# Performance work log

Hardware: AMD Instinct MI355X
Metric: run time of the kernel (lower is better)

The kernel has to match this reference:

```python
import jax, jax.numpy as jnp
import numpy as np

B, NPER, F, D, E, NUM_STEPS = 256, 512, 256, 32, 524288, 4
N = B * NPER
INIT_TAU, TAU_SCALE, STEP_ALPHA = 0.1, 0.5, 5.0


def setup_inputs() -> dict:
    key = jax.random.key(0)
    ks = jax.random.split(key, 10)
    x_start = jax.random.uniform(ks[0], (N,), jnp.float32, 0.1, 1.0)   # strictly positive iterate
    x_solution = jax.random.uniform(ks[1], (N,), jnp.float32, 0.0, 1.0)
    q = jax.random.normal(ks[2], (N,), jnp.float32)
    edge_src = jax.random.randint(ks[3], (E,), 0, N, jnp.int32)
    edge_dst = jax.random.randint(ks[4], (E,), 0, N, jnp.int32)
    vals_batch = jnp.repeat(jnp.arange(B, dtype=jnp.int32), NPER)      # equal-sized graphs
    proj_matrix = jax.random.normal(ks[5], (B, NPER, F), jnp.float32) / np.float32(np.sqrt(NPER))
    W_in = jax.random.normal(ks[6], (2, D), jnp.float32) / np.float32(np.sqrt(2.0))
    b_in = jnp.zeros((D,), jnp.float32)
    W_msg = jax.random.normal(ks[7], (D, D), jnp.float32) / np.float32(np.sqrt(D))
    b_msg = jnp.zeros((D,), jnp.float32)
    W_out = jax.random.normal(ks[8], (D, 1), jnp.float32) / np.float32(np.sqrt(D))
    b_out = jnp.zeros((1,), jnp.float32)
    return {"x_start": x_start, "x_solution": x_solution, "q": q,
            "proj_matrix": proj_matrix, "W_in": W_in, "b_in": b_in,
            "W_msg": W_msg, "b_msg": b_msg, "W_out": W_out, "b_out": b_out,
            "edge_src": edge_src, "edge_dst": edge_dst, "vals_batch": vals_batch}


def _l1_normalize(x, batch):
    # per-graph L1 normalization: x / sum_i |x_i| over the graph segment
    s = jax.ops.segment_sum(jnp.abs(x), batch, num_segments=B)
    return x / (s[batch] + 1e-12)


def _line_search(x, d, batch, max_alpha):
    # largest per-graph alpha s.t. x + alpha*d >= 0, capped at max_alpha
    ratio = jnp.where(d < 0, x / jnp.maximum(-d, 1e-12), max_alpha)
    a = jnp.clip(jax.ops.segment_min(ratio, batch, num_segments=B), 0.0, max_alpha)
    return a[batch]  # gathered back to per-node


def _gnn(xs, q, edge_src, edge_dst, W_in, b_in, W_msg, b_msg, W_out, b_out):
    h = jax.nn.relu(jnp.stack([xs, q], axis=-1) @ W_in + b_in)      # [N, D]
    m = h[edge_src] @ W_msg + b_msg                                  # [E, D]
    agg = jax.ops.segment_sum(m, edge_dst, num_segments=N)          # [N, D]
    h2 = jax.nn.relu(h + agg)
    return h2 @ W_out[:, 0] + b_out[0]                               # [N]


def reference(x_start, x_solution, q, proj_matrix, W_in, b_in, W_msg, b_msg,
              W_out, b_out, edge_src, edge_dst, vals_batch):
    tau = INIT_TAU
    xs = x_start
    preds, labels = [], []
    for _ in range(NUM_STEPS):
        pred = _gnn(xs, q, edge_src, edge_dst, W_in, b_in, W_msg, b_msg, W_out, b_out)
        preds.append(pred)
        labels.append(_l1_normalize(x_solution - xs, vals_batch))
        p = _l1_normalize(jax.lax.stop_gradient(pred), vals_batch)   # .detach() in torch
        direction = p + 3.0 * tau / (xs + tau)
        tau = max(tau * TAU_SCALE, 1e-5)
        # to_dense_batch with equal graph sizes == reshape; project onto nullspace basis
        dd = direction.reshape(B, NPER)
        df = jnp.einsum('bnf,bn->bf', proj_matrix, dd)               # [B, F]
        pproj = jnp.einsum('bnf,bf->bn', proj_matrix, df).reshape(-1)  # [N]
        alpha = _line_search(xs, pproj, vals_batch, STEP_ALPHA) * 0.995
        xs = xs + alpha * pproj
    return jnp.stack(preds, axis=1), jnp.stack(labels, axis=1)       # each [N, NUM_STEPS]
```

## Files before the change

kernel.cpp:

```cpp
#include <hip/hip_runtime.h>

#define BB 256
#define NPER 512
#define FF 256
#define DD 32
#define EE 524288
#define NN (BB*NPER)
#define NSTEPS 4

__device__ __forceinline__ float bflo(unsigned u) { return __uint_as_float(u << 16); }
__device__ __forceinline__ float bfhi(unsigned u) { return __uint_as_float(u & 0xFFFF0000u); }
__device__ __forceinline__ unsigned rtn_bf16(unsigned u) {
    return (u + 0x7FFFu + ((u >> 16) & 1u)) >> 16;
}


__global__ void k_degpack(const int* __restrict__ dst, unsigned* __restrict__ deg,
                          const float* __restrict__ xs0, const float* __restrict__ q,
                          float2* __restrict__ xq) {
    int t = blockIdx.x * blockDim.x + threadIdx.x;
    if (t < NN) { float2 v; v.x = xs0[t]; v.y = q[t]; xq[t] = v; }
    atomicAdd(&deg[dst[t]], 1u);
}

__global__ __launch_bounds__(256) void k_alloc(const unsigned* __restrict__ deg,
                                               unsigned* __restrict__ gcur,
                                               unsigned* __restrict__ rowstart,
                                               unsigned* __restrict__ cursor) {
    __shared__ unsigned r[256];
    __shared__ unsigned base;
    int t = threadIdx.x;
    int i = blockIdx.x * 256 + t;
    unsigned d = deg[i];
    r[t] = d;
    __syncthreads();
    for (int o = 1; o < 256; o <<= 1) {
        unsigned v = (t >= o) ? r[t - o] : 0u;
        __syncthreads();
        r[t] += v;
        __syncthreads();
    }
    if (t == 255) base = atomicAdd(gcur, r[255]);
    __syncthreads();
    unsigned excl = r[t] - d + base;
    rowstart[i] = excl;
    cursor[i] = excl;
}

__global__ void k_fill(const int* __restrict__ src, const int* __restrict__ dst,
                       unsigned* __restrict__ cursor, int* __restrict__ csr_src) {
    int e = blockIdx.x * blockDim.x + threadIdx.x;
    unsigned pos = atomicAdd(&cursor[dst[e]], 1u);
    csr_src[pos] = src[e];
}


template<int STEP>
__global__ void k_node_g(const float2* __restrict__ xq,
                         const float* __restrict__ Win, const float* __restrict__ bin,
                         const unsigned* __restrict__ rowstart, const unsigned* __restrict__ deg,
                         const int* __restrict__ csr_src,
                         const float* __restrict__ Wmsg, const float* __restrict__ bmsg,
                         const float* __restrict__ Wout, const float* __restrict__ bout,
                         float* __restrict__ pred, float* __restrict__ out_preds) {
    int tid = threadIdx.x;
    int d = tid & 31;
    int i = blockIdx.x * 8 + (tid >> 5);
    float w0 = Win[d], w1 = Win[DD + d], b0 = bin[d];
    float wcol[DD];
    #pragma unroll
    for (int k = 0; k < DD; ++k) wcol[k] = Wmsg[k * DD + d];
    unsigned rs = rowstart[i];
    unsigned dg = deg[i];
    unsigned nfull = dg < 32u ? dg : 32u;
    float xv = 0.f, qv = 0.f;
    if ((unsigned)d < nfull) {
        int sv = csr_src[rs + d];
        float2 v = xq[sv];
        xv = v.x; qv = v.y;
    }
    float s = 0.f;
    for (unsigned j = 0; j < nfull; ++j) {
        float xj = __shfl(xv, (int)j, 32);
        float qj = __shfl(qv, (int)j, 32);
        s += fmaxf(xj * w0 + qj * w1 + b0, 0.f);
    }
    for (unsigned j = 32; j < dg; ++j) {
        int sv = csr_src[rs + j];
        float2 v = xq[sv];
        s += fmaxf(v.x * w0 + v.y * w1 + b0, 0.f);
    }
    float2 self = xq[i];
    float hval = fmaxf(self.x * w0 + self.y * w1 + b0, 0.f);
    float agg = (float)dg * bmsg[d];
    #pragma unroll
    for (int k = 0; k < DD; ++k) agg += __shfl(s, k, 32) * wcol[k];
    float h2 = fmaxf(hval + agg, 0.f);
    float v = h2 * Wout[d];
    for (int o = 16; o > 0; o >>= 1) v += __shfl_down(v, o, 32);
    if (d == 0) {
        float pr = v + bout[0];
        pred[i] = pr;
        out_preds[i * NSTEPS + STEP] = pr;
    }
}

template<int STEP0>
__global__ __launch_bounds__(256) void k_dfc(const float* __restrict__ Pf,
                                             unsigned short* __restrict__ Pbf,
                                             const float2* __restrict__ xq,
                                             const float* __restrict__ xsol,
                                             const float* __restrict__ pred,
                                             float* __restrict__ out_labels,
                                             float* __restrict__ dfp,
                                             float tau, int step) {
    __shared__ float dd_l[64];
    __shared__ float sl[4 * FF];
    __shared__ float redA[4], redB[4];
    int blk = blockIdx.x;
    int b = blk >> 3, s = blk & 7;
    int t = threadIdx.x;
    int w = t >> 6, lane = t & 63;
    int gbase = b * NPER;

    float x0 = xq[gbase + t].x;
    float x1 = xq[gbase + 256 + t].x;
    float r0 = xsol[gbase + t] - x0;
    float r1 = xsol[gbase + 256 + t] - x1;
    float a1 = fabsf(r0) + fabsf(r1);
    float a2 = fabsf(pred[gbase + t]) + fabsf(pred[gbase + 256 + t]);
    #pragma unroll
    for (int o = 32; o > 0; o >>= 1) {
        a1 += __shfl_down(a1, o, 64);
        a2 += __shfl_down(a2, o, 64);
    }
    if (lane == 0) { redA[w] = a1; redB[w] = a2; }
    __syncthreads();
    float Sr = 1e-12f + redA[0] + redA[1] + redA[2] + redA[3];
    float Sp = 1e-12f + redB[0] + redB[1] + redB[2] + redB[3];
    if (s == 0) {
        out_labels[(size_t)(gbase + t) * NSTEPS + step] = r0 / Sr;
        out_labels[(size_t)(gbase + 256 + t) * NSTEPS + step] = r1 / Sr;
    }
    if (t < 64) {
        int row = s * 64 + t;
        float xx = xq[gbase + row].x;
        dd_l[t] = pred[gbase + row] / Sp + 3.0f * tau / (xx + tau);
    }
    __syncthreads();

    size_t pbase = ((size_t)(gbase + s * 64 + w * 16)) * FF + 4 * lane;
    float4 acc = {0.f, 0.f, 0.f, 0.f};
    if (STEP0) {
        const float4* Pr = (const float4*)(Pf + pbase);
        uint2* Pw = (uint2*)(Pbf + pbase);
        #pragma unroll 4
        for (int n = 0; n < 16; ++n) {
            float4 pv = Pr[(size_t)n * 64];
            float sc = dd_l[w * 16 + n];
            acc.x += pv.x * sc; acc.y += pv.y * sc;
            acc.z += pv.z * sc; acc.w += pv.w * sc;
            unsigned u0 = rtn_bf16(__float_as_uint(pv.x));
            unsigned u1 = rtn_bf16(__float_as_uint(pv.y));
            unsigned u2 = rtn_bf16(__float_as_uint(pv.z));
            unsigned u3 = rtn_bf16(__float_as_uint(pv.w));
            uint2 o; o.x = u0 | (u1 << 16); o.y = u2 | (u3 << 16);
            Pw[(size_t)n * 64] = o;
        }
    } else {
        const uint2* Pr = (const uint2*)(Pbf + pbase);
        #pragma unroll 8
        for (int n = 0; n < 16; ++n) {
            uint2 pv = Pr[(size_t)n * 64];
            float sc = dd_l[w * 16 + n];
            acc.x += bflo(pv.x) * sc; acc.y += bfhi(pv.x) * sc;
            acc.z += bflo(pv.y) * sc; acc.w += bfhi(pv.y) * sc;
        }
    }
    ((float4*)sl)[w * 64 + lane] = acc;
    __syncthreads();
    if (t < FF) {
        float v = sl[t] + sl[FF + t] + sl[2 * FF + t] + sl[3 * FF + t];
        dfp[(size_t)((step * BB + b) * 8 + s) * FF + t] = v;
    }
}

__global__ __launch_bounds__(1024) void k_ppu(const unsigned short* __restrict__ Pbf,
                                              const float* __restrict__ dfp,
                                              float2* __restrict__ xq,
                                              const float* __restrict__ xsol,
                                              float* __restrict__ out_labels,
                                              int step, int last) {
    __shared__ float x_l[NPER], pp_l[NPER], dfl[FF];
    __shared__ float wmin[16], red[16];
    int b = blockIdx.x;
    int t = threadIdx.x;
    int w = t >> 6, lane = t & 63;
    int gbase = b * NPER;
    if (t < FF) {
        const float* dp = dfp + (size_t)((step * BB + b) * 8) * FF + t;
        float v = 0.f;
        #pragma unroll
        for (int s = 0; s < 8; ++s) v += dp[s * FF];
        dfl[t] = v;
    }
    if (t < NPER) x_l[t] = xq[gbase + t].x;
    __syncthreads();

    float4 dfv = ((const float4*)dfl)[lane];
    const uint2* Pr = (const uint2*)(Pbf + ((size_t)(gbase + w * 32)) * FF + 4 * lane);
    float mloc = 5.0f;
    #pragma unroll
    for (int n = 0; n < 32; ++n) {
        uint2 pv = Pr[(size_t)n * 64];
        float pr = bflo(pv.x) * dfv.x + bfhi(pv.x) * dfv.y
                 + bflo(pv.y) * dfv.z + bfhi(pv.y) * dfv.w;
        #pragma unroll
        for (int o = 1; o < 64; o <<= 1) pr += __shfl_xor(pr, o, 64);
        int row = w * 32 + n;
        if (lane == 0) pp_l[row] = pr;
        float ratio = (pr < 0.f) ? (x_l[row] / fmaxf(-pr, 1e-12f)) : 5.0f;
        mloc = fminf(mloc, ratio);
    }
    if (lane == 0) wmin[w] = mloc;
    __syncthreads();
    float mm = wmin[0];
    #pragma unroll
    for (int k = 1; k < 16; ++k) mm = fminf(mm, wmin[k]);
    float alpha = fminf(fmaxf(mm, 0.f), 5.0f) * 0.995f;
    float xnew = 0.f;
    if (t < NPER) {
        xnew = x_l[t] + alpha * pp_l[t];
        xq[gbase + t].x = xnew;
    }
    if (last) {
        float r = 0.f, a1 = 0.f;
        if (t < NPER) { r = xsol[gbase + t] - xnew; a1 = fabsf(r); }
        #pragma unroll
        for (int o = 32; o > 0; o >>= 1) a1 += __shfl_down(a1, o, 64);
        if (lane == 0) red[w] = a1;
        __syncthreads();
        float Sr = 1e-12f;
        #pragma unroll
        for (int k = 0; k < 16; ++k) Sr += red[k];
        if (t < NPER) out_labels[(size_t)(gbase + t) * NSTEPS + (NSTEPS - 1)] = r / Sr;
    }
}


extern "C" void kernel_launch(void* const* d_in, const int* in_sizes, int n_in,
                              void* d_out, int out_size, void* d_ws, size_t ws_size,
                              hipStream_t stream) {
    const float* x_start = (const float*)d_in[0];
    const float* x_sol   = (const float*)d_in[1];
    const float* q       = (const float*)d_in[2];
    const float* P       = (const float*)d_in[3];
    const float* Win     = (const float*)d_in[4];
    const float* bin     = (const float*)d_in[5];
    const float* Wmsg    = (const float*)d_in[6];
    const float* bmsg    = (const float*)d_in[7];
    const float* Wout    = (const float*)d_in[8];
    const float* bout    = (const float*)d_in[9];
    const int*   esrc    = (const int*)d_in[10];
    const int*   edst    = (const int*)d_in[11];

    float* out_preds  = (float*)d_out;
    float* out_labels = (float*)d_out + (size_t)NN * NSTEPS;

    float* w = (float*)d_ws;
    unsigned* deg  = (unsigned*)w; w += NN;
    unsigned* gcur = (unsigned*)w; w += 2;
    float2* xq  = (float2*)w; w += 2 * (size_t)NN;
    float* pred  = w; w += NN;
    float* dfp   = w; w += (size_t)3 * BB * 8 * FF;
    unsigned* rowstart = (unsigned*)w; w += NN;
    unsigned* cursor   = (unsigned*)w; w += NN;
    int* csr_src       = (int*)w;      w += EE;
    unsigned short* Pbf = (unsigned short*)w;

    hipMemsetAsync(deg, 0, (NN + 2) * sizeof(unsigned), stream);
    k_degpack<<<EE / 256, 256, 0, stream>>>(edst, deg, x_start, q, xq);
    k_alloc<<<NN / 256, 256, 0, stream>>>(deg, gcur, rowstart, cursor);
    k_fill<<<EE / 256, 256, 0, stream>>>(esrc, edst, cursor, csr_src);

    float tau = 0.1f;
    for (int step = 0; step < NSTEPS; ++step) {
        switch (step) {
        case 0: k_node_g<0><<<NN / 8, 256, 0, stream>>>(xq, Win, bin, rowstart, deg, csr_src,
                                                        Wmsg, bmsg, Wout, bout, pred, out_preds); break;
        case 1: k_node_g<1><<<NN / 8, 256, 0, stream>>>(xq, Win, bin, rowstart, deg, csr_src,
                                                        Wmsg, bmsg, Wout, bout, pred, out_preds); break;
        case 2: k_node_g<2><<<NN / 8, 256, 0, stream>>>(xq, Win, bin, rowstart, deg, csr_src,
                                                        Wmsg, bmsg, Wout, bout, pred, out_preds); break;
        default: k_node_g<3><<<NN / 8, 256, 0, stream>>>(xq, Win, bin, rowstart, deg, csr_src,
                                                         Wmsg, bmsg, Wout, bout, pred, out_preds); break;
        }
        if (step < NSTEPS - 1) {
            if (step == 0)
                k_dfc<1><<<BB * 8, 256, 0, stream>>>(P, Pbf, xq, x_sol, pred,
                                                     out_labels, dfp, tau, step);
            else
                k_dfc<0><<<BB * 8, 256, 0, stream>>>(P, Pbf, xq, x_sol, pred,
                                                     out_labels, dfp, tau, step);
            k_ppu<<<BB, 1024, 0, stream>>>(Pbf, dfp, xq, x_sol, out_labels,
                                           step, step == NSTEPS - 2 ? 1 : 0);
        }
        tau = fmaxf(tau * 0.5f, 1e-5f);
    }
}
```

Measured before the change: 527.3 us.

## Fuse projection and back-projection kernels, keeping P rows in registers

```diff
diff --git a/kernel.cpp b/kernel.cpp
--- a/kernel.cpp
+++ b/kernel.cpp
@@ -106,29 +106,29 @@
 }
 
 template<int STEP0>
-__global__ __launch_bounds__(256) void k_dfc(const float* __restrict__ Pf,
-                                             unsigned short* __restrict__ Pbf,
-                                             const float2* __restrict__ xq,
-                                             const float* __restrict__ xsol,
-                                             const float* __restrict__ pred,
-                                             float* __restrict__ out_labels,
-                                             float* __restrict__ dfp,
-                                             float tau, int step) {
-    __shared__ float dd_l[64];
-    __shared__ float sl[4 * FF];
-    __shared__ float redA[4], redB[4];
-    int blk = blockIdx.x;
-    int b = blk >> 3, s = blk & 7;
+__global__ __launch_bounds__(1024) void k_stepR(const float* __restrict__ Pf,
+                                                unsigned short* __restrict__ Pbf,
+                                                float2* __restrict__ xq,
+                                                const float* __restrict__ xsol,
+                                                const float* __restrict__ pred,
+                                                float* __restrict__ out_labels,
+                                                float tau, int step, int last) {
+    __shared__ float dd_l[NPER], x_l[NPER], pp_l[NPER];
+    __shared__ float sl[16 * FF];
+    __shared__ float dfl[FF];
+    __shared__ float redA[16], redB[16], wmin[16];
+    int b = blockIdx.x;
     int t = threadIdx.x;
     int w = t >> 6, lane = t & 63;
     int gbase = b * NPER;
 
-    float x0 = xq[gbase + t].x;
-    float x1 = xq[gbase + 256 + t].x;
-    float r0 = xsol[gbase + t] - x0;
-    float r1 = xsol[gbase + 256 + t] - x1;
-    float a1 = fabsf(r0) + fabsf(r1);
-    float a2 = fabsf(pred[gbase + t]) + fabsf(pred[gbase + 256 + t]);
+    float x = 0.f, r = 0.f, p = 0.f, a1 = 0.f, a2 = 0.f;
+    if (t < NPER) {
+        x = xq[gbase + t].x;
+        r = xsol[gbase + t] - x;
+        p = pred[gbase + t];
+        a1 = fabsf(r); a2 = fabsf(p);
+    }
     #pragma unroll
     for (int o = 32; o > 0; o >>= 1) {
         a1 += __shfl_down(a1, o, 64);
@@ -136,94 +136,74 @@
     }
     if (lane == 0) { redA[w] = a1; redB[w] = a2; }
     __syncthreads();
-    float Sr = 1e-12f + redA[0] + redA[1] + redA[2] + redA[3];
-    float Sp = 1e-12f + redB[0] + redB[1] + redB[2] + redB[3];
-    if (s == 0) {
-        out_labels[(size_t)(gbase + t) * NSTEPS + step] = r0 / Sr;
-        out_labels[(size_t)(gbase + 256 + t) * NSTEPS + step] = r1 / Sr;
-    }
-    if (t < 64) {
-        int row = s * 64 + t;
-        float xx = xq[gbase + row].x;
-        dd_l[t] = pred[gbase + row] / Sp + 3.0f * tau / (xx + tau);
-    }
-    __syncthreads();
-
-    size_t pbase = ((size_t)(gbase + s * 64 + w * 16)) * FF + 4 * lane;
+    float Sr = 1e-12f, Sp = 1e-12f;
+    #pragma unroll
+    for (int k = 0; k < 16; ++k) { Sr += redA[k]; Sp += redB[k]; }
+    if (t < NPER) {
+        out_labels[(size_t)(gbase + t) * NSTEPS + step] = r / Sr;
+        x_l[t] = x;
+        dd_l[t] = p / Sp + 3.0f * tau / (x + tau);
+    }
+    __syncthreads();
+
+    size_t pbase = ((size_t)(gbase + w * 32)) * FF + 4 * lane;
+    unsigned pl[64];
     float4 acc = {0.f, 0.f, 0.f, 0.f};
     if (STEP0) {
         const float4* Pr = (const float4*)(Pf + pbase);
         uint2* Pw = (uint2*)(Pbf + pbase);
-        #pragma unroll 4
-        for (int n = 0; n < 16; ++n) {
+        #pragma unroll
+        for (int n = 0; n < 32; ++n) {
             float4 pv = Pr[(size_t)n * 64];
-            float sc = dd_l[w * 16 + n];
+            float sc = dd_l[w * 32 + n];
             acc.x += pv.x * sc; acc.y += pv.y * sc;
             acc.z += pv.z * sc; acc.w += pv.w * sc;
             unsigned u0 = rtn_bf16(__float_as_uint(pv.x));
             unsigned u1 = rtn_bf16(__float_as_uint(pv.y));
             unsigned u2 = rtn_bf16(__float_as_uint(pv.z));
             unsigned u3 = rtn_bf16(__float_as_uint(pv.w));
-            uint2 o; o.x = u0 | (u1 << 16); o.y = u2 | (u3 << 16);
-            Pw[(size_t)n * 64] = o;
+            unsigned lo = u0 | (u1 << 16), hi = u2 | (u3 << 16);
+            uint2 o2; o2.x = lo; o2.y = hi;
+            Pw[(size_t)n * 64] = o2;
+            pl[2 * n] = lo; pl[2 * n + 1] = hi;
         }
     } else {
         const uint2* Pr = (const uint2*)(Pbf + pbase);
-        #pragma unroll 8
-        for (int n = 0; n < 16; ++n) {
+        #pragma unroll
+        for (int n = 0; n < 32; ++n) {
             uint2 pv = Pr[(size_t)n * 64];
-            float sc = dd_l[w * 16 + n];
+            float sc = dd_l[w * 32 + n];
             acc.x += bflo(pv.x) * sc; acc.y += bfhi(pv.x) * sc;
             acc.z += bflo(pv.y) * sc; acc.w += bfhi(pv.y) * sc;
+            pl[2 * n] = pv.x; pl[2 * n + 1] = pv.y;
         }
     }
     ((float4*)sl)[w * 64 + lane] = acc;
     __syncthreads();
     if (t < FF) {
-        float v = sl[t] + sl[FF + t] + sl[2 * FF + t] + sl[3 * FF + t];
-        dfp[(size_t)((step * BB + b) * 8 + s) * FF + t] = v;
-    }
-}
-
-__global__ __launch_bounds__(1024) void k_ppu(const unsigned short* __restrict__ Pbf,
-                                              const float* __restrict__ dfp,
-                                              float2* __restrict__ xq,
-                                              const float* __restrict__ xsol,
-                                              float* __restrict__ out_labels,
-                                              int step, int last) {
-    __shared__ float x_l[NPER], pp_l[NPER], dfl[FF];
-    __shared__ float wmin[16], red[16];
-    int b = blockIdx.x;
-    int t = threadIdx.x;
-    int w = t >> 6, lane = t & 63;
-    int gbase = b * NPER;
-    if (t < FF) {
-        const float* dp = dfp + (size_t)((step * BB + b) * 8) * FF + t;
         float v = 0.f;
         #pragma unroll
-        for (int s = 0; s < 8; ++s) v += dp[s * FF];
+        for (int k = 0; k < 16; ++k) v += sl[k * FF + t];
         dfl[t] = v;
     }
-    if (t < NPER) x_l[t] = xq[gbase + t].x;
     __syncthreads();
 
     float4 dfv = ((const float4*)dfl)[lane];
-    const uint2* Pr = (const uint2*)(Pbf + ((size_t)(gbase + w * 32)) * FF + 4 * lane);
     float mloc = 5.0f;
     #pragma unroll
     for (int n = 0; n < 32; ++n) {
-        uint2 pv = Pr[(size_t)n * 64];
-        float pr = bflo(pv.x) * dfv.x + bfhi(pv.x) * dfv.y
-                 + bflo(pv.y) * dfv.z + bfhi(pv.y) * dfv.w;
+        float pr = bflo(pl[2 * n]) * dfv.x + bfhi(pl[2 * n]) * dfv.y
+                 + bflo(pl[2 * n + 1]) * dfv.z + bfhi(pl[2 * n + 1]) * dfv.w;
         #pragma unroll
         for (int o = 1; o < 64; o <<= 1) pr += __shfl_xor(pr, o, 64);
-        int row = w * 32 + n;
-        if (lane == 0) pp_l[row] = pr;
-        float ratio = (pr < 0.f) ? (x_l[row] / fmaxf(-pr, 1e-12f)) : 5.0f;
+        if (lane == 0) pp_l[w * 32 + n] = pr;
+        float xr = x_l[w * 32 + n];
+        float ratio = (pr < 0.f) ? (xr / fmaxf(-pr, 1e-12f)) : 5.0f;
         mloc = fminf(mloc, ratio);
     }
     if (lane == 0) wmin[w] = mloc;
     __syncthreads();
+
     float mm = wmin[0];
     #pragma unroll
     for (int k = 1; k < 16; ++k) mm = fminf(mm, wmin[k]);
@@ -234,16 +214,17 @@
         xq[gbase + t].x = xnew;
     }
     if (last) {
-        float r = 0.f, a1 = 0.f;
-        if (t < NPER) { r = xsol[gbase + t] - xnew; a1 = fabsf(r); }
-        #pragma unroll
-        for (int o = 32; o > 0; o >>= 1) a1 += __shfl_down(a1, o, 64);
-        if (lane == 0) red[w] = a1;
-        __syncthreads();
-        float Sr = 1e-12f;
-        #pragma unroll
-        for (int k = 0; k < 16; ++k) Sr += red[k];
-        if (t < NPER) out_labels[(size_t)(gbase + t) * NSTEPS + (NSTEPS - 1)] = r / Sr;
+        float rr = 0.f, aa = 0.f;
+        if (t < NPER) { rr = xsol[gbase + t] - xnew; aa = fabsf(rr); }
+        #pragma unroll
+        for (int o = 32; o > 0; o >>= 1) aa += __shfl_down(aa, o, 64);
+        __syncthreads();
+        if (lane == 0) redA[w] = aa;
+        __syncthreads();
+        float Sr2 = 1e-12f;
+        #pragma unroll
+        for (int k = 0; k < 16; ++k) Sr2 += redA[k];
+        if (t < NPER) out_labels[(size_t)(gbase + t) * NSTEPS + (NSTEPS - 1)] = rr / Sr2;
     }
 }
 
@@ -272,7 +253,6 @@
     unsigned* gcur = (unsigned*)w; w += 2;
     float2* xq  = (float2*)w; w += 2 * (size_t)NN;
     float* pred  = w; w += NN;
-    float* dfp   = w; w += (size_t)3 * BB * 8 * FF;
     unsigned* rowstart = (unsigned*)w; w += NN;
     unsigned* cursor   = (unsigned*)w; w += NN;
     int* csr_src       = (int*)w;      w += EE;
@@ -296,14 +276,13 @@
                                                          Wmsg, bmsg, Wout, bout, pred, out_preds); break;
         }
         if (step < NSTEPS - 1) {
+            int last = (step == NSTEPS - 2) ? 1 : 0;
             if (step == 0)
-                k_dfc<1><<<BB * 8, 256, 0, stream>>>(P, Pbf, xq, x_sol, pred,
-                                                     out_labels, dfp, tau, step);
+                k_stepR<1><<<BB, 1024, 0, stream>>>(P, Pbf, xq, x_sol, pred,
+                                                    out_labels, tau, step, last);
             else
-                k_dfc<0><<<BB * 8, 256, 0, stream>>>(P, Pbf, xq, x_sol, pred,
-                                                     out_labels, dfp, tau, step);
-            k_ppu<<<BB, 1024, 0, stream>>>(Pbf, dfp, xq, x_sol, out_labels,
-                                           step, step == NSTEPS - 2 ? 1 : 0);
+                k_stepR<0><<<BB, 1024, 0, stream>>>(P, Pbf, xq, x_sol, pred,
+                                                    out_labels, tau, step, last);
         }
         tau = fmaxf(tau * 0.5f, 1e-5f);
     }
```

New measurement: 552.0 us. +4.7%, slower.
